# Performance work log

Hardware: AMD Instinct MI355X
Metric: run time of the kernel (lower is better)

The kernel has to match this reference:

```python
import jax, jax.numpy as jnp
import numpy as np

K = 16  # num neighbors


def setup_inputs() -> dict:
    key = jax.random.key(0)
    ks = jax.random.split(key, 10)
    B, N, d_in, d_out = 4, 8192, 64, 128
    h = d_out // 2
    return {
        "xyz": jax.random.normal(ks[0], (B, 3, N), jnp.float32),
        "feature": jax.random.normal(ks[1], (B, d_in, N), jnp.float32),
        "w1": jax.random.normal(ks[2], (h, 10), jnp.float32) * 0.1,
        "b1": jax.random.normal(ks[3], (h,), jnp.float32) * 0.1,
        "w2": jax.random.normal(ks[4], (h, h), jnp.float32) * 0.1,
        "b2": jax.random.normal(ks[5], (h,), jnp.float32) * 0.1,
        "w3": jax.random.normal(ks[6], (h, h), jnp.float32) * 0.1,
        "b3": jax.random.normal(ks[7], (h,), jnp.float32) * 0.1,
        "ws": jax.random.normal(ks[8], (d_out, d_in), jnp.float32) * 0.1,
        "bs": jax.random.normal(ks[9], (d_out,), jnp.float32) * 0.1,
    }


def reference(xyz, feature, w1, b1, w2, b2, w3, b3, ws, bs):
    # xyz: [B,3,N], feature: [B,d_in,N]
    xyz_t = jnp.transpose(xyz, (0, 2, 1))  # [B,N,3]
    sq = jnp.sum(xyz_t * xyz_t, axis=-1)  # [B,N]
    # squared pairwise distance [B,N,N]
    dist = sq[:, :, None] + sq[:, None, :] - 2.0 * jnp.einsum("bnc,bmc->bnm", xyz_t, xyz_t)
    _, idx = jax.lax.top_k(-dist, K)  # smallest-k -> [B,N,K]
    # gather neighbor coords: [B,N,K,3]
    knn_xyz = jax.vmap(lambda pts, ind: pts[ind])(xyz_t, idx)
    center = jnp.broadcast_to(xyz_t[:, :, None, :], knn_xyz.shape)  # [B,N,K,3]
    diff = knn_xyz - center
    dsq = jnp.sum(diff * diff, axis=-1, keepdims=True)  # [B,N,K,1]
    pos = jnp.concatenate([center, knn_xyz, diff, dsq], axis=-1)  # [B,N,K,10]
    # three 1x1 convs over channel dim (no activations, faithful to source)
    h = jnp.einsum("bnkc,oc->bnko", pos, w1) + b1
    h = jnp.einsum("bnkc,oc->bnko", h, w2) + b2
    h = jnp.einsum("bnkc,oc->bnko", h, w3) + b3
    fe = jnp.max(h, axis=2)  # max-pool over neighbors -> [B,N,d_out//2]
    fe = jnp.transpose(fe, (0, 2, 1))  # [B,d_out//2,N]
    shortcut = jnp.einsum("bcn,oc->bon", feature, ws) + bs[None, :, None]
    return jnp.concatenate([fe, fe], axis=1) + shortcut  # [B,d_out,N]
```

## Files before the change

kernel.cpp:

```cpp
#include <hip/hip_runtime.h>

#define B_ 4
#define N_ 8192
#define DIN 64
#define HDIM 64
#define DOUT 128
#define KNN 16
#define QPB 64
#define PART 8
#define NTHR (QPB * PART)
#define CHUNK (N_ / PART)
#define CAP 16
#define CAPP 17
#define BLOCKS_PER_B (N_ / QPB)

__global__ __launch_bounds__(256) void k_prep(
    const float* __restrict__ xyz,
    const float* __restrict__ w1, const float* __restrict__ b1,
    const float* __restrict__ w2, const float* __restrict__ b2,
    const float* __restrict__ w3, const float* __restrict__ b3,
    float4* __restrict__ pk, float4* __restrict__ prm) {
  const int blk = blockIdx.x, t = threadIdx.x;
  const int b = blk >> 5;
  const int m = ((blk & 31) << 8) + t;
  const float* xb = xyz + (size_t)b * 3 * N_;
  float x = xb[m], y = xb[N_ + m], z = xb[2 * N_ + m];
  float sq = __fadd_rn(__fadd_rn(__fmul_rn(x, x), __fmul_rn(y, y)), __fmul_rn(z, z));
  pk[((size_t)b << 13) + m] = make_float4(x, y, z, sq);

  if (blk == 0) {
    __shared__ float M2[HDIM][10];
    __shared__ float bb[HDIM];
    const int o = t;
    if (o < HDIM) {
      float r[10];
#pragma unroll
      for (int c = 0; c < 10; c++) r[c] = 0.f;
      float s = b2[o];
      for (int l = 0; l < HDIM; l++) {
        float w = w2[o * HDIM + l];
#pragma unroll
        for (int c = 0; c < 10; c++) r[c] = fmaf(w, w1[l * 10 + c], r[c]);
        s = fmaf(w, b1[l], s);
      }
#pragma unroll
      for (int c = 0; c < 10; c++) M2[o][c] = r[c];
      bb[o] = s;
    }
    __syncthreads();
    if (o < HDIM) {
      float r3[10];
#pragma unroll
      for (int c = 0; c < 10; c++) r3[c] = 0.f;
      float bc = b3[o];
      for (int l = 0; l < HDIM; l++) {
        float w = w3[o * HDIM + l];
#pragma unroll
        for (int c = 0; c < 10; c++) r3[c] = fmaf(w, M2[l][c], r3[c]);
        bc = fmaf(w, bb[l], bc);
      }
      prm[o]      = make_float4(r3[0] - r3[6], r3[1] - r3[7], r3[2] - r3[8], bc);
      prm[64 + o] = make_float4(r3[3] + r3[6], r3[4] + r3[7], r3[5] + r3[8], r3[9]);
    }
  }
}

#define MAX16(VARR, VMAX)                                                     \
  {                                                                           \
    float _m0 = fmaxf(fmaxf(VARR[0], VARR[1]), VARR[2]);                      \
    float _m1 = fmaxf(fmaxf(VARR[3], VARR[4]), VARR[5]);                      \
    float _m2 = fmaxf(fmaxf(VARR[6], VARR[7]), VARR[8]);                      \
    float _m3 = fmaxf(fmaxf(VARR[9], VARR[10]), VARR[11]);                    \
    float _m4 = fmaxf(fmaxf(VARR[12], VARR[13]), VARR[14]);                   \
    float _a = fmaxf(fmaxf(_m0, _m1), _m2);                                   \
    float _b = fmaxf(fmaxf(_m3, _m4), VARR[15]);                              \
    VMAX = fmaxf(_a, _b);                                                     \
  }

#define INSERT16(VARR, IARR, VMAX, DVAL, MIDX)                    \
  {                                                               \
    bool done = false;                                            \
    _Pragma("unroll") for (int _i = 0; _i < KNN; _i++) {          \
      bool hit = (!done) && (VARR[_i] == VMAX);                   \
      if (hit) { VARR[_i] = (DVAL); IARR[_i] = (MIDX); }          \
      done = done | hit;                                          \
    }                                                             \
    MAX16(VARR, VMAX);                                            \
  }

#define FLUSH()                                                   \
  {                                                               \
    for (int c_ = 0; c_ < cnt; c_++) {                            \
      float fd_ = poolF[lbase + c_];                              \
      int fm_ = poolI[lbase + c_];                                \
      if (fd_ < vmax) { INSERT16(v, id, vmax, fd_, fm_); }        \
    }                                                             \
    cnt = 0;                                                      \
    atomicMin(&tau[q], __float_as_uint(vmax));                    \
    gate = fminf(vmax, __uint_as_float(tau[q]));                  \
  }

__global__ __launch_bounds__(NTHR, 4) void k_knn_fe(
    const float4* __restrict__ pk, const float4* __restrict__ prm,
    const float* __restrict__ feature, const float* __restrict__ wsM,
    const float* __restrict__ bs, float* __restrict__ out) {
  const int blk = blockIdx.x;
  const int b  = blk / BLOCKS_PER_B;
  const int n0 = (blk % BLOCKS_PER_B) * QPB;
  const int t = threadIdx.x;
  const int q = t & 63;
  const int j = __builtin_amdgcn_readfirstlane(t >> 6);
  const int lbase = t * CAPP;

  __shared__ unsigned tau[QPB];
  __shared__ float4 prmL[2 * HDIM];
  __shared__ alignas(16) float poolF[CAPP * NTHR];
  __shared__ alignas(16) unsigned short poolI[CAPP * NTHR];

  if (t < QPB) tau[t] = 0x7f800000u;
  for (int i = t; i < 2 * HDIM; i += NTHR) prmL[i] = prm[i];

  const float4 qv = pk[((size_t)b << 13) + n0 + q];
  const float qx = qv.x, qy = qv.y, qz = qv.z, qs = qv.w;

  const float INF = __uint_as_float(0x7f800000u);
  float v[KNN]; int id[KNN];
  float vmax, gate;
  int cnt = 0;
  __syncthreads();

  const float4* pj = pk + ((size_t)b << 13) + j * CHUNK;

  {
    float4 c[KNN];
#pragma unroll
    for (int e = 0; e < KNN; e++) c[e] = pj[e];
#pragma unroll
    for (int e = 0; e < KNN; e++) {
      float dot = fmaf(c[e].z, qz, fmaf(c[e].y, qy, __fmul_rn(c[e].x, qx)));
      v[e] = fmaf(-2.0f, dot, __fadd_rn(qs, c[e].w));
      id[e] = j * CHUNK + e;
    }
    MAX16(v, vmax);
    atomicMin(&tau[q], __float_as_uint(vmax));
    gate = fminf(vmax, __uint_as_float(tau[q]));
  }

  unsigned tnext = tau[q];
  for (int u0 = KNN; u0 < CHUNK; u0 += 8) {
    if (__any(cnt > CAP - 8)) { FLUSH(); }
    gate = fminf(gate, __uint_as_float(tnext));
    tnext = tau[q];
    float4 c[8];
#pragma unroll
    for (int e = 0; e < 8; e++) c[e] = pj[u0 + e];
#pragma unroll
    for (int e = 0; e < 8; e++) {
      float dot = fmaf(c[e].z, qz, fmaf(c[e].y, qy, __fmul_rn(c[e].x, qx)));
      float d = fmaf(-2.0f, dot, __fadd_rn(qs, c[e].w));
      if (d < gate) {
        poolF[lbase + cnt] = d;
        poolI[lbase + cnt] = (unsigned short)(j * CHUNK + u0 + e);
        cnt++;
      }
    }
  }
  FLUSH();
  __syncthreads();

#pragma unroll
  for (int i = 0; i < KNN; i++) {
    poolF[(j * KNN + i) * QPB + q] = v[i];
    poolI[(j * KNN + i) * QPB + q] = (unsigned short)id[i];
  }
  __syncthreads();

  float fv[KNN]; int fid[KNN]; float fm = INF;
  if (j < 4) {
    const int l0 = (2 * j) * KNN, r1 = (2 * j + 1) * KNN;
#pragma unroll
    for (int i = 0; i < KNN; i++) {
      fv[i] = poolF[(l0 + i) * QPB + q];
      fid[i] = poolI[(l0 + i) * QPB + q];
    }
    MAX16(fv, fm);
    for (int s = 0; s < KNN; s++) {
      float d = poolF[(r1 + s) * QPB + q];
      if (d < fm) { int m_ = poolI[(r1 + s) * QPB + q]; INSERT16(fv, fid, fm, d, m_); }
    }
#pragma unroll
    for (int i = 0; i < KNN; i++) {
      poolF[(l0 + i) * QPB + q] = fv[i];
      poolI[(l0 + i) * QPB + q] = (unsigned short)fid[i];
    }
  }
  __syncthreads();
  if (j < 2) {
    const int l0 = (4 * j) * KNN, r1 = (4 * j + 2) * KNN;
#pragma unroll
    for (int i = 0; i < KNN; i++) {
      fv[i] = poolF[(l0 + i) * QPB + q];
      fid[i] = poolI[(l0 + i) * QPB + q];
    }
    MAX16(fv, fm);
    for (int s = 0; s < KNN; s++) {
      float d = poolF[(r1 + s) * QPB + q];
      if (d < fm) { int m_ = poolI[(r1 + s) * QPB + q]; INSERT16(fv, fid, fm, d, m_); }
    }
#pragma unroll
    for (int i = 0; i < KNN; i++) {
      poolF[(l0 + i) * QPB + q] = fv[i];
      poolI[(l0 + i) * QPB + q] = (unsigned short)fid[i];
    }
  }
  __syncthreads();
  if (j == 0) {
#pragma unroll
    for (int i = 0; i < KNN; i++) {
      fv[i] = poolF[i * QPB + q];
      fid[i] = poolI[i * QPB + q];
    }
    MAX16(fv, fm);
    for (int s = 0; s < KNN; s++) {
      float d = poolF[(4 * KNN + s) * QPB + q];
      if (d < fm) { int m_ = poolI[(4 * KNN + s) * QPB + q]; INSERT16(fv, fid, fm, d, m_); }
    }
#pragma unroll
    for (int i = 0; i < KNN; i++) poolI[i * QPB + q] = (unsigned short)fid[i];
  }
  __syncthreads();

#pragma unroll
  for (int kk = 0; kk < 2; kk++) {
    int k = j * 2 + kk;
    int m = poolI[k * QPB + q];
    float4 c = pk[((size_t)b << 13) + m];
    float dx = __fsub_rn(c.x, qx), dy = __fsub_rn(c.y, qy), dz = __fsub_rn(c.z, qz);
    float dsq = __fadd_rn(__fadd_rn(__fmul_rn(dx, dx), __fmul_rn(dy, dy)),
                          __fmul_rn(dz, dz));
    poolF[k * QPB + q] = c.x;
    poolF[(KNN + k) * QPB + q] = c.y;
    poolF[(2 * KNN + k) * QPB + q] = c.z;
    poolF[(3 * KNN + k) * QPB + q] = dsq;
  }
  __syncthreads();

  float fo[8];
  {
    float nx[KNN], ny[KNN], nz[KNN], nd[KNN];
#pragma unroll
    for (int k = 0; k < KNN; k++) {
      nx[k] = poolF[k * QPB + q];
      ny[k] = poolF[(KNN + k) * QPB + q];
      nz[k] = poolF[(2 * KNN + k) * QPB + q];
      nd[k] = poolF[(3 * KNN + k) * QPB + q];
    }
#pragma unroll
    for (int oi = 0; oi < 8; oi++) {
      int o = j * 8 + oi;
      float4 pA = prmL[o], pB = prmL[HDIM + o];
      float basev = fmaf(qz, pA.z, fmaf(qy, pA.y, fmaf(qx, pA.x, pA.w)));
      float mx = -INF;
#pragma unroll
      for (int k = 0; k < KNN; k++) {
        float tv = fmaf(nz[k], pB.z,
                   fmaf(ny[k], pB.y,
                   fmaf(nx[k], pB.x, __fmul_rn(nd[k], pB.w))));
        mx = fmaxf(mx, tv);
      }
      fo[oi] = basev + mx;
    }
  }
  __syncthreads();

  float* wsL = poolF;
  float* feL = (float*)poolI;
  for (int i = t; i < DOUT * DIN; i += NTHR) wsL[i] = wsM[i];
#pragma unroll
  for (int r = 0; r < 8; r++) {
    int c = j * 8 + r;
    feL[c * QPB + q] = feature[(size_t)(b * DIN + c) * N_ + n0 + q];
  }
  __syncthreads();

  float acc[16];
#pragma unroll
  for (int oi = 0; oi < 16; oi++) acc[oi] = 0.f;
  for (int c4 = 0; c4 < DIN / 4; c4++) {
    float f0 = feL[(4 * c4 + 0) * QPB + q];
    float f1 = feL[(4 * c4 + 1) * QPB + q];
    float f2 = feL[(4 * c4 + 2) * QPB + q];
    float f3 = feL[(4 * c4 + 3) * QPB + q];
#pragma unroll
    for (int oi = 0; oi < 16; oi++) {
      int o = (oi < 8) ? (j * 8 + oi) : (64 + j * 8 + oi - 8);
      float4 w = ((const float4*)(wsL + o * DIN))[c4];
      acc[oi] = fmaf(w.x, f0, acc[oi]);
      acc[oi] = fmaf(w.y, f1, acc[oi]);
      acc[oi] = fmaf(w.z, f2, acc[oi]);
      acc[oi] = fmaf(w.w, f3, acc[oi]);
    }
  }
  float* ob = out + (size_t)b * DOUT * N_ + n0 + q;
#pragma unroll
  for (int oi = 0; oi < 16; oi++) {
    int o = (oi < 8) ? (j * 8 + oi) : (64 + j * 8 + oi - 8);
    ob[(size_t)o * N_] = acc[oi] + bs[o] + fo[oi & 7];
  }
}

extern "C" void kernel_launch(void* const* d_in, const int* in_sizes, int n_in,
                              void* d_out, int out_size, void* d_ws, size_t ws_size,
                              hipStream_t stream) {
  const float* xyz     = (const float*)d_in[0];
  const float* feature = (const float*)d_in[1];
  const float* w1 = (const float*)d_in[2];
  const float* b1 = (const float*)d_in[3];
  const float* w2 = (const float*)d_in[4];
  const float* b2 = (const float*)d_in[5];
  const float* w3 = (const float*)d_in[6];
  const float* b3 = (const float*)d_in[7];
  const float* wsM = (const float*)d_in[8];
  const float* bs  = (const float*)d_in[9];
  float* out = (float*)d_out;

  float4* prm = (float4*)d_ws;
  float4* pkB = (float4*)((char*)d_ws + 8192);

  hipLaunchKernelGGL(k_prep, dim3(128), dim3(256), 0, stream,
                     xyz, w1, b1, w2, b2, w3, b3, pkB, prm);
  hipLaunchKernelGGL(k_knn_fe, dim3(B_ * BLOCKS_PER_B), dim3(NTHR), 0, stream,
                     pkB, prm, feature, wsM, bs, out);
}
```

Measured before the change: 274.3 us.

## Use margin-gated cheap distance filter with prefetched candidates and exact refetch on flush

```diff
diff --git a/kernel.cpp b/kernel.cpp
--- a/kernel.cpp
+++ b/kernel.cpp
@@ -13,6 +13,7 @@
 #define CAP 16
 #define CAPP 17
 #define BLOCKS_PER_B (N_ / QPB)
+#define GMARGIN 1e-3f
 
 __global__ __launch_bounds__(256) void k_prep(
     const float* __restrict__ xyz,
@@ -88,16 +89,40 @@
     MAX16(VARR, VMAX);                                            \
   }
 
-#define FLUSH()                                                   \
-  {                                                               \
-    for (int c_ = 0; c_ < cnt; c_++) {                            \
-      float fd_ = poolF[lbase + c_];                              \
-      int fm_ = poolI[lbase + c_];                                \
-      if (fd_ < vmax) { INSERT16(v, id, vmax, fd_, fm_); }        \
-    }                                                             \
-    cnt = 0;                                                      \
-    atomicMin(&tau[q], __float_as_uint(vmax));                    \
-    gate = fminf(vmax, __uint_as_float(tau[q]));                  \
+#define FLUSH()                                                               \
+  {                                                                           \
+    _Pragma("unroll") for (int c0_ = 0; c0_ < CAP; c0_ += 8) {                \
+      int mi_[8]; float4 fc_[8];                                              \
+      _Pragma("unroll") for (int e_ = 0; e_ < 8; e_++)                        \
+        mi_[e_] = poolI[lbase + c0_ + e_] & (N_ - 1);                         \
+      _Pragma("unroll") for (int e_ = 0; e_ < 8; e_++)                        \
+        fc_[e_] = pk[bb + mi_[e_]];                                           \
+      _Pragma("unroll") for (int e_ = 0; e_ < 8; e_++) {                      \
+        if (c0_ + e_ < cnt) {                                                 \
+          float dot_ = fmaf(fc_[e_].z, qz,                                    \
+                       fmaf(fc_[e_].y, qy, __fmul_rn(fc_[e_].x, qx)));        \
+          float d_ = fmaf(-2.0f, dot_, __fadd_rn(qs, fc_[e_].w));             \
+          if (d_ < vmax) { INSERT16(v, id, vmax, d_, mi_[e_]); }              \
+        }                                                                     \
+      }                                                                       \
+    }                                                                         \
+    cnt = 0;                                                                  \
+    unsigned old_ = atomicMin(&tau[q], __float_as_uint(vmax));                \
+    gate = fminf(vmax, __uint_as_float(old_));                                \
+    G = __fadd_rn(__fsub_rn(gate, qs), GMARGIN);                              \
+  }
+
+#define PROC8(CARR, U0)                                                       \
+  {                                                                           \
+    if (__any(cnt > CAP - 8)) { FLUSH(); }                                    \
+    _Pragma("unroll") for (int e = 0; e < 8; e++) {                           \
+      float gg = fmaf(CARR[e].x, nx2, fmaf(CARR[e].y, ny2,                    \
+                  fmaf(CARR[e].z, nz2, CARR[e].w)));                          \
+      if (gg < G) {                                                           \
+        poolI[lbase + cnt] = (unsigned short)(jC + (U0) + e);                 \
+        cnt++;                                                                \
+      }                                                                       \
+    }                                                                         \
   }
 
 __global__ __launch_bounds__(NTHR, 4) void k_knn_fe(
@@ -111,25 +136,28 @@
   const int q = t & 63;
   const int j = __builtin_amdgcn_readfirstlane(t >> 6);
   const int lbase = t * CAPP;
+  const size_t bb = (size_t)b << 13;
 
   __shared__ unsigned tau[QPB];
   __shared__ float4 prmL[2 * HDIM];
-  __shared__ alignas(16) float poolF[CAPP * NTHR];
+  __shared__ alignas(16) float poolF[128 * QPB];
   __shared__ alignas(16) unsigned short poolI[CAPP * NTHR];
 
   if (t < QPB) tau[t] = 0x7f800000u;
   for (int i = t; i < 2 * HDIM; i += NTHR) prmL[i] = prm[i];
 
-  const float4 qv = pk[((size_t)b << 13) + n0 + q];
+  const float4 qv = pk[bb + n0 + q];
   const float qx = qv.x, qy = qv.y, qz = qv.z, qs = qv.w;
+  const float nx2 = -2.0f * qx, ny2 = -2.0f * qy, nz2 = -2.0f * qz;
 
   const float INF = __uint_as_float(0x7f800000u);
   float v[KNN]; int id[KNN];
-  float vmax, gate;
+  float vmax, gate, G;
   int cnt = 0;
   __syncthreads();
 
-  const float4* pj = pk + ((size_t)b << 13) + j * CHUNK;
+  const float4* pj = pk + bb + (size_t)j * CHUNK;
+  const int jC = j * CHUNK;
 
   {
     float4 c[KNN];
@@ -139,30 +167,25 @@
     for (int e = 0; e < KNN; e++) {
       float dot = fmaf(c[e].z, qz, fmaf(c[e].y, qy, __fmul_rn(c[e].x, qx)));
       v[e] = fmaf(-2.0f, dot, __fadd_rn(qs, c[e].w));
-      id[e] = j * CHUNK + e;
+      id[e] = jC + e;
     }
     MAX16(v, vmax);
-    atomicMin(&tau[q], __float_as_uint(vmax));
-    gate = fminf(vmax, __uint_as_float(tau[q]));
-  }
-
-  unsigned tnext = tau[q];
-  for (int u0 = KNN; u0 < CHUNK; u0 += 8) {
-    if (__any(cnt > CAP - 8)) { FLUSH(); }
-    gate = fminf(gate, __uint_as_float(tnext));
-    tnext = tau[q];
-    float4 c[8];
-#pragma unroll
-    for (int e = 0; e < 8; e++) c[e] = pj[u0 + e];
-#pragma unroll
-    for (int e = 0; e < 8; e++) {
-      float dot = fmaf(c[e].z, qz, fmaf(c[e].y, qy, __fmul_rn(c[e].x, qx)));
-      float d = fmaf(-2.0f, dot, __fadd_rn(qs, c[e].w));
-      if (d < gate) {
-        poolF[lbase + cnt] = d;
-        poolI[lbase + cnt] = (unsigned short)(j * CHUNK + u0 + e);
-        cnt++;
-      }
+    unsigned old = atomicMin(&tau[q], __float_as_uint(vmax));
+    gate = fminf(vmax, __uint_as_float(old));
+    G = __fadd_rn(__fsub_rn(gate, qs), GMARGIN);
+  }
+
+  {
+    float4 ca[8], cb[8];
+#pragma unroll
+    for (int e = 0; e < 8; e++) ca[e] = pj[KNN + e];
+    for (int u0 = KNN; u0 < CHUNK; u0 += 16) {
+#pragma unroll
+      for (int e = 0; e < 8; e++) cb[e] = pj[u0 + 8 + e];
+      PROC8(ca, u0);
+#pragma unroll
+      for (int e = 0; e < 8; e++) ca[e] = pj[u0 + 16 + e];
+      PROC8(cb, u0 + 8);
     }
   }
   FLUSH();
@@ -234,7 +257,7 @@
   for (int kk = 0; kk < 2; kk++) {
     int k = j * 2 + kk;
     int m = poolI[k * QPB + q];
-    float4 c = pk[((size_t)b << 13) + m];
+    float4 c = pk[bb + m];
     float dx = __fsub_rn(c.x, qx), dy = __fsub_rn(c.y, qy), dz = __fsub_rn(c.z, qz);
     float dsq = __fadd_rn(__fadd_rn(__fmul_rn(dx, dx), __fmul_rn(dy, dy)),
                           __fmul_rn(dz, dz));
```

Result: faster. 263.3 us (-4.0%).

## Double-buffer candidate point loads with inline-asm prefetch in KNN scan

Applied to the files above, without the earlier changes.

```diff
diff --git a/kernel.cpp b/kernel.cpp
--- a/kernel.cpp
+++ b/kernel.cpp
@@ -14,6 +14,8 @@
 #define CAPP 17
 #define BLOCKS_PER_B (N_ / QPB)
 
+typedef float f32x4 __attribute__((ext_vector_type(4)));
+
 __global__ __launch_bounds__(256) void k_prep(
     const float* __restrict__ xyz,
     const float* __restrict__ w1, const float* __restrict__ b1,
@@ -96,8 +98,39 @@
       if (fd_ < vmax) { INSERT16(v, id, vmax, fd_, fm_); }        \
     }                                                             \
     cnt = 0;                                                      \
-    atomicMin(&tau[q], __float_as_uint(vmax));                    \
-    gate = fminf(vmax, __uint_as_float(tau[q]));                  \
+    unsigned old_ = atomicMin(&tau[q], __float_as_uint(vmax));    \
+    gate = fminf(vmax, __uint_as_float(old_));                    \
+  }
+
+#define ISSUE6(C, VO)                                                         \
+  {                                                                           \
+    unsigned vo_ = (VO);                                                      \
+    asm volatile(                                                             \
+        "global_load_dwordx4 %0, %6, %7 offset:0\n\t"                         \
+        "global_load_dwordx4 %1, %6, %7 offset:16\n\t"                        \
+        "global_load_dwordx4 %2, %6, %7 offset:32\n\t"                        \
+        "global_load_dwordx4 %3, %6, %7 offset:48\n\t"                        \
+        "global_load_dwordx4 %4, %6, %7 offset:64\n\t"                        \
+        "global_load_dwordx4 %5, %6, %7 offset:80"                            \
+        : "=&v"(C[0]), "=&v"(C[1]), "=&v"(C[2]),                              \
+          "=&v"(C[3]), "=&v"(C[4]), "=&v"(C[5])                               \
+        : "v"(vo_), "s"(pj));                                                 \
+  }
+
+#define CONSUME6(C, U0, NWAIT)                                                \
+  {                                                                           \
+    if (__any(cnt > CAP - 6)) { FLUSH(); }                                    \
+    asm volatile("s_waitcnt vmcnt(" #NWAIT ")" ::: "memory");                 \
+    __builtin_amdgcn_sched_barrier(0);                                        \
+    _Pragma("unroll") for (int e = 0; e < 6; e++) {                           \
+      float dot_ = fmaf(C[e].z, qz, fmaf(C[e].y, qy, __fmul_rn(C[e].x, qx))); \
+      float d_ = fmaf(-2.0f, dot_, __fadd_rn(qs, C[e].w));                    \
+      if (d_ < gate) {                                                        \
+        poolF[lbase + cnt] = d_;                                              \
+        poolI[lbase + cnt] = (unsigned short)(jC + (U0) + e);                 \
+        cnt++;                                                                \
+      }                                                                       \
+    }                                                                         \
   }
 
 __global__ __launch_bounds__(NTHR, 4) void k_knn_fe(
@@ -111,6 +144,7 @@
   const int q = t & 63;
   const int j = __builtin_amdgcn_readfirstlane(t >> 6);
   const int lbase = t * CAPP;
+  const size_t bb = (size_t)b << 13;
 
   __shared__ unsigned tau[QPB];
   __shared__ float4 prmL[2 * HDIM];
@@ -120,7 +154,7 @@
   if (t < QPB) tau[t] = 0x7f800000u;
   for (int i = t; i < 2 * HDIM; i += NTHR) prmL[i] = prm[i];
 
-  const float4 qv = pk[((size_t)b << 13) + n0 + q];
+  const float4 qv = pk[bb + n0 + q];
   const float qx = qv.x, qy = qv.y, qz = qv.z, qs = qv.w;
 
   const float INF = __uint_as_float(0x7f800000u);
@@ -129,7 +163,12 @@
   int cnt = 0;
   __syncthreads();
 
-  const float4* pj = pk + ((size_t)b << 13) + j * CHUNK;
+  const float4* pj = pk + bb + (size_t)j * CHUNK;
+  const int jC = j * CHUNK;
+
+  f32x4 cA[6], cB[6];
+  ISSUE6(cA, 16u * 16u);
+  ISSUE6(cB, 22u * 16u);
 
   {
     float4 c[KNN];
@@ -139,31 +178,24 @@
     for (int e = 0; e < KNN; e++) {
       float dot = fmaf(c[e].z, qz, fmaf(c[e].y, qy, __fmul_rn(c[e].x, qx)));
       v[e] = fmaf(-2.0f, dot, __fadd_rn(qs, c[e].w));
-      id[e] = j * CHUNK + e;
+      id[e] = jC + e;
     }
     MAX16(v, vmax);
-    atomicMin(&tau[q], __float_as_uint(vmax));
-    gate = fminf(vmax, __uint_as_float(tau[q]));
-  }
-
-  unsigned tnext = tau[q];
-  for (int u0 = KNN; u0 < CHUNK; u0 += 8) {
-    if (__any(cnt > CAP - 8)) { FLUSH(); }
-    gate = fminf(gate, __uint_as_float(tnext));
-    tnext = tau[q];
-    float4 c[8];
-#pragma unroll
-    for (int e = 0; e < 8; e++) c[e] = pj[u0 + e];
-#pragma unroll
-    for (int e = 0; e < 8; e++) {
-      float dot = fmaf(c[e].z, qz, fmaf(c[e].y, qy, __fmul_rn(c[e].x, qx)));
-      float d = fmaf(-2.0f, dot, __fadd_rn(qs, c[e].w));
-      if (d < gate) {
-        poolF[lbase + cnt] = d;
-        poolI[lbase + cnt] = (unsigned short)(j * CHUNK + u0 + e);
-        cnt++;
-      }
-    }
+    unsigned old = atomicMin(&tau[q], __float_as_uint(vmax));
+    gate = fminf(vmax, __uint_as_float(old));
+  }
+
+  {
+    int u0 = 16;
+    for (int i = 0; i < 83; i++) {
+      CONSUME6(cA, u0, 6);
+      ISSUE6(cA, (unsigned)((u0 + 12) * 16));
+      CONSUME6(cB, u0 + 6, 6);
+      ISSUE6(cB, (unsigned)((u0 + 18) * 16));
+      u0 += 12;
+    }
+    CONSUME6(cA, u0, 6);
+    CONSUME6(cB, u0 + 6, 0);
   }
   FLUSH();
   __syncthreads();
@@ -234,7 +266,7 @@
   for (int kk = 0; kk < 2; kk++) {
     int k = j * 2 + kk;
     int m = poolI[k * QPB + q];
-    float4 c = pk[((size_t)b << 13) + m];
+    float4 c = pk[bb + m];
     float dx = __fsub_rn(c.x, qx), dy = __fsub_rn(c.y, qy), dz = __fsub_rn(c.z, qz);
     float dsq = __fadd_rn(__fadd_rn(__fmul_rn(dx, dx), __fmul_rn(dy, dy)),
                           __fmul_rn(dz, dz));
```

New measurement: 291.4 us. 6.2% more time.
